# Optimization experiments

Hardware: AMD Instinct MI355X
Metric: run time of the kernel (lower is better)

## Reference

```python
import jax, jax.numpy as jnp
import numpy as np

B, LTMS, TTS, C_IN, F, H = 64, 16, 256, 128, 256, 256


def setup_inputs() -> dict:
    key = jax.random.key(0)
    ks = jax.random.split(key, 6)
    s = 0.05  # small init keeps relu-GRU numerically tame
    return {
        "x": jax.random.normal(ks[0], (B, LTMS * TTS, C_IN), dtype=jnp.float32),
        "conv_w": jax.random.normal(ks[1], (1, C_IN, F), dtype=jnp.float32) * s,
        "conv_b": jnp.zeros((F,), dtype=jnp.float32),
        "attn_w": jax.random.normal(ks[2], (TTS, TTS), dtype=jnp.float32) * s,
        "attn_b": jnp.zeros((TTS,), dtype=jnp.float32),
        "gru_w": jax.random.normal(ks[3], (F, 3 * H), dtype=jnp.float32) * s,
        "gru_u": jax.random.normal(ks[4], (H, 3 * H), dtype=jnp.float32) * s,
        "gru_b": jnp.zeros((2, 3 * H), dtype=jnp.float32),
    }


def _forward(x, conv_w, conv_b, attn_w, attn_b, gru_w, gru_u, gru_b):
    b = x.shape[0]
    # [B, LTMS*TTS, C] -> [B*LTMS, TTS, C]; segments are independent, so the
    # original per-segment Python loop vectorizes into the leading batch dim.
    xs = x.reshape(b * LTMS, TTS, C_IN)
    # Conv1D kernel_size=1 == pointwise GEMM, then ReLU (dropout=0 at inference)
    conv = jax.nn.relu(jnp.einsum('ntc,cf->ntf', xs, conv_w[0]) + conv_b)  # [N,T,F]
    # Attention: softmax(Dense) over time axis per filter, multiply back
    xt = conv.transpose(0, 2, 1)                                  # [N,F,T]
    probs = jax.nn.softmax(xt @ attn_w + attn_b, axis=-1)         # [N,F,T]
    x_att = conv * probs.transpose(0, 2, 1)                       # [N,T,F]
    # GRU (keras v2, reset_after=True), activation=relu, gate order z,r,h
    bi, br = gru_b[0], gru_b[1]
    gates_x = x_att @ gru_w + bi                                  # [N,T,3H]
    def step(h, gx):
        rec = h @ gru_u + br
        xz, xr, xh = jnp.split(gx, 3, axis=-1)
        rz, rr, rh = jnp.split(rec, 3, axis=-1)
        z = jax.nn.sigmoid(xz + rz)
        r = jax.nn.sigmoid(xr + rr)
        hh = jax.nn.relu(xh + r * rh)
        h_new = z * h + (1.0 - z) * hh
        return h_new, None
    h0 = jnp.zeros((b * LTMS, H), dtype=x.dtype)
    h_final, _ = jax.lax.scan(step, h0, gates_x.transpose(1, 0, 2))
    return h_final.reshape(b, LTMS, H)


def reference(x, conv_w, conv_b, attn_w, attn_b, gru_w, gru_u, gru_b):
    return _forward(x, conv_w, conv_b, attn_w, attn_b, gru_w, gru_u, gru_b)
```

## Files before the change

kernel.cpp:

```cpp
#include <hip/hip_runtime.h>
#include <stdint.h>

typedef unsigned short u16;
typedef __attribute__((ext_vector_type(8))) __bf16 bf16x8;
typedef __attribute__((ext_vector_type(8))) u16 u16x8;
typedef __attribute__((ext_vector_type(4))) float f32x4;

#define TTS 256
#define NSEG 1024
#define TC 32

__device__ __forceinline__ u16 f2bf(float f) {
  union { float f; uint32_t u; } v; v.f = f;
  uint32_t r = v.u + 0x7fffu + ((v.u >> 16) & 1u);
  return (u16)(r >> 16);
}
__device__ __forceinline__ float bf2f(u16 h) {
  union { uint32_t u; float f; } v; v.u = ((uint32_t)h) << 16;
  return v.f;
}
__device__ __forceinline__ float sigm(float x) {
  return __builtin_amdgcn_rcpf(1.0f + __expf(-x));
}
__device__ __forceinline__ void gl16(const void* g, void* l) {
  __builtin_amdgcn_global_load_lds(
      (const __attribute__((address_space(1))) unsigned int*)g,
      (__attribute__((address_space(3))) unsigned int*)l, 16, 0, 0);
}

__global__ void k_transp4(const float* __restrict__ cw, const float* __restrict__ aw,
                          const float* __restrict__ gw, const float* __restrict__ gu,
                          u16* __restrict__ cwT, u16* __restrict__ awT,
                          u16* __restrict__ gwT, u16* __restrict__ guT) {
  int b = blockIdx.x;
  const float* in; u16* out; int R, C, base;
  if (b < 128)       { in = cw; out = cwT; R = 128; C = 256; base = 0; }
  else if (b < 384)  { in = aw; out = awT; R = 256; C = 256; base = 128; }
  else if (b < 1152) { in = gw; out = gwT; R = 256; C = 768; base = 384; }
  else               { in = gu; out = guT; R = 256; C = 768; base = 1152; }
  int i = (b - base) * 256 + threadIdx.x;
  if (i < R * C) {
    int r = i / C, c = i % C;
    out[(size_t)c * R + r] = f2bf(in[i]);
  }
}

template <bool RELU, bool STORE_T, int AMODE>
__global__ __launch_bounds__(512, 2) void k_gemm(
    const void* __restrict__ Av, const u16* __restrict__ Bt,
    const float* __restrict__ bias, u16* __restrict__ out, int K, int Nld, int t0) {
  __shared__ __attribute__((aligned(16))) u16 ldsA[2][4096];
  __shared__ __attribute__((aligned(16))) u16 ldsB[2][8192];
  const int tid  = threadIdx.x;
  const int w    = tid >> 6;
  const int lane = tid & 63;
  const int quad = lane >> 4;
  const int l16  = lane & 15;
  const int m0 = blockIdx.x * 128;
  const int n0 = blockIdx.y * 256;
  const int wm = w >> 2, wn = w & 3;
  const int arow = tid & 127, ac = tid >> 7;
  const float* Af = (const float*)Av;
  const u16*   Ax = (const u16*)Av;

  f32x4 acc[4][4];
#pragma unroll
  for (int i = 0; i < 4; i++)
#pragma unroll
    for (int j = 0; j < 4; j++) acc[i][j] = f32x4{0.f, 0.f, 0.f, 0.f};

  float4 p0, p1;
  if (AMODE == 0) {
    const float* p = Af + (size_t)(m0 + arow) * K + ac * 8;
    p0 = *(const float4*)p;
    p1 = *(const float4*)(p + 4);
  } else {
    int r = m0 + arow, kk = ac * 8;
    gl16(Ax + (size_t)(r >> 5) * 65536 + (size_t)(kk >> 6) * 16384 +
             (t0 + (r & 31)) * 64 + (kk & 63),
         &ldsA[0][tid * 8]);
  }
#pragma unroll
  for (int i = 0; i < 2; i++) {
    int idx = i * 512 + tid, brow = idx & 255, bc = idx >> 8;
    gl16(Bt + (size_t)(n0 + brow) * K + bc * 8, &ldsB[0][idx * 8]);
  }
  if (AMODE == 0) {
    *(ushort4*)&ldsA[0][tid * 8]     = ushort4{f2bf(p0.x), f2bf(p0.y), f2bf(p0.z), f2bf(p0.w)};
    *(ushort4*)&ldsA[0][tid * 8 + 4] = ushort4{f2bf(p1.x), f2bf(p1.y), f2bf(p1.z), f2bf(p1.w)};
  }
  __syncthreads();

  int cur = 0;
  for (int k0 = 0; k0 < K; k0 += 32) {
    const int kn = k0 + 32;
    const bool more = kn < K;
    float4 q0, q1;
    if (more) {
      if (AMODE == 0) {
        const float* p = Af + (size_t)(m0 + arow) * K + kn + ac * 8;
        q0 = *(const float4*)p;
        q1 = *(const float4*)(p + 4);
      } else {
        int r = m0 + arow, kk = kn + ac * 8;
        gl16(Ax + (size_t)(r >> 5) * 65536 + (size_t)(kk >> 6) * 16384 +
                 (t0 + (r & 31)) * 64 + (kk & 63),
             &ldsA[cur ^ 1][tid * 8]);
      }
#pragma unroll
      for (int i = 0; i < 2; i++) {
        int idx = i * 512 + tid, brow = idx & 255, bc = idx >> 8;
        gl16(Bt + (size_t)(n0 + brow) * K + kn + bc * 8, &ldsB[cur ^ 1][idx * 8]);
      }
    }
    bf16x8 a[4], b[4];
#pragma unroll
    for (int i = 0; i < 4; i++)
      a[i] = *(const bf16x8*)&ldsA[cur][(quad * 128 + wm * 64 + i * 16 + l16) * 8];
#pragma unroll
    for (int j = 0; j < 4; j++)
      b[j] = *(const bf16x8*)&ldsB[cur][(quad * 256 + wn * 64 + j * 16 + l16) * 8];
#pragma unroll
    for (int i = 0; i < 4; i++)
#pragma unroll
      for (int j = 0; j < 4; j++)
        acc[i][j] = __builtin_amdgcn_mfma_f32_16x16x32_bf16(a[i], b[j], acc[i][j], 0, 0, 0);
    if (AMODE == 0 && more) {
      *(ushort4*)&ldsA[cur ^ 1][tid * 8]     = ushort4{f2bf(q0.x), f2bf(q0.y), f2bf(q0.z), f2bf(q0.w)};
      *(ushort4*)&ldsA[cur ^ 1][tid * 8 + 4] = ushort4{f2bf(q1.x), f2bf(q1.y), f2bf(q1.z), f2bf(q1.w)};
    }
    __syncthreads();
    cur ^= 1;
  }

#pragma unroll
  for (int j = 0; j < 4; j++) {
    int col = n0 + wn * 64 + j * 16 + l16;
    float bv = bias[col];
#pragma unroll
    for (int i = 0; i < 4; i++) {
      int row0 = m0 + wm * 64 + i * 16 + quad * 4;
      if (STORE_T) {
        int nseg = row0 >> 8, tt0 = row0 & 255;
        ushort4 o;
        float v0 = acc[i][j][0] + bv, v1 = acc[i][j][1] + bv;
        float v2 = acc[i][j][2] + bv, v3 = acc[i][j][3] + bv;
        if (RELU) {
          v0 = fmaxf(v0, 0.f); v1 = fmaxf(v1, 0.f);
          v2 = fmaxf(v2, 0.f); v3 = fmaxf(v3, 0.f);
        }
        o.x = f2bf(v0); o.y = f2bf(v1); o.z = f2bf(v2); o.w = f2bf(v3);
        *(ushort4*)&out[(size_t)nseg * 65536 + (size_t)(col >> 6) * 16384 +
                        (col & 63) * 256 + tt0] = o;
      } else {
#pragma unroll
        for (int r = 0; r < 4; r++) {
          float v = acc[i][j][r] + bv;
          if (RELU) v = fmaxf(v, 0.f);
          out[(size_t)(row0 + r) * Nld + col] = f2bf(v);
        }
      }
    }
  }
}

__global__ __launch_bounds__(256, 3) void k_attn(
    u16* xac,
    const u16* __restrict__ Wt,
    const float* __restrict__ attn_b) {
  __shared__ u16 ldsC[16384];
  __shared__ float redmax[4][64];
  __shared__ float redsum[4][64];
  __shared__ __attribute__((aligned(16))) u16 xbuf[4][16][76];
  const int tid  = threadIdx.x;
  const int w    = tid >> 6;
  const int lane = tid & 63;
  const int quad = lane >> 4;
  const int l16  = lane & 15;
  const int seg = blockIdx.x;
  const int c4  = blockIdx.y;
  u16* reg = xac + (size_t)seg * 65536 + (size_t)c4 * 16384;

  {
    const int f = tid & 63, g = tid >> 6;
#pragma unroll
    for (int u = 0; u < 8; u++) {
      int tch = g * 8 + u;
      *(bf16x8*)&ldsC[(tch * 64 + f) * 8] =
          *(const bf16x8*)(reg + (size_t)f * 256 + tch * 8);
    }
  }
  __syncthreads();

  f32x4 acc[4][4];
#pragma unroll
  for (int i = 0; i < 4; i++)
#pragma unroll
    for (int j = 0; j < 4; j++) acc[i][j] = f32x4{0.f, 0.f, 0.f, 0.f};

#pragma unroll
  for (int s = 0; s < 8; s++) {
    int k0 = s * 32;
    bf16x8 a[4], b[4];
#pragma unroll
    for (int i = 0; i < 4; i++)
      a[i] = *(const bf16x8*)(Wt + (size_t)(w * 64 + i * 16 + l16) * 256 + k0 + quad * 8);
#pragma unroll
    for (int j = 0; j < 4; j++)
      b[j] = *(const bf16x8*)&ldsC[((s * 4 + quad) * 64 + j * 16 + l16) * 8];
#pragma unroll
    for (int i = 0; i < 4; i++)
#pragma unroll
      for (int j = 0; j < 4; j++)
        acc[i][j] = __builtin_amdgcn_mfma_f32_16x16x32_bf16(a[i], b[j], acc[i][j], 0, 0, 0);
  }

#pragma unroll
  for (int i = 0; i < 4; i++)
#pragma unroll
    for (int r = 0; r < 4; r++) {
      float ab = attn_b[w * 64 + i * 16 + quad * 4 + r];
#pragma unroll
      for (int j = 0; j < 4; j++) acc[i][j][r] += ab;
    }

  float lmax[4];
#pragma unroll
  for (int j = 0; j < 4; j++) {
    float m = -1e30f;
#pragma unroll
    for (int i = 0; i < 4; i++)
#pragma unroll
      for (int r = 0; r < 4; r++) m = fmaxf(m, acc[i][j][r]);
    m = fmaxf(m, __shfl_xor(m, 16));
    m = fmaxf(m, __shfl_xor(m, 32));
    lmax[j] = m;
  }
  if (quad == 0) {
#pragma unroll
    for (int j = 0; j < 4; j++) redmax[w][j * 16 + l16] = lmax[j];
  }
  __syncthreads();
  float gmax[4];
#pragma unroll
  for (int j = 0; j < 4; j++) {
    int c = j * 16 + l16;
    gmax[j] = fmaxf(fmaxf(redmax[0][c], redmax[1][c]), fmaxf(redmax[2][c], redmax[3][c]));
  }
  float lsum[4];
#pragma unroll
  for (int j = 0; j < 4; j++) {
    float sacc = 0.f;
#pragma unroll
    for (int i = 0; i < 4; i++)
#pragma unroll
      for (int r = 0; r < 4; r++) {
        float e = __expf(acc[i][j][r] - gmax[j]);
        acc[i][j][r] = e;
        sacc += e;
      }
    sacc += __shfl_xor(sacc, 16);
    sacc += __shfl_xor(sacc, 32);
    lsum[j] = sacc;
  }
  if (quad == 0) {
#pragma unroll
    for (int j = 0; j < 4; j++) redsum[w][j * 16 + l16] = lsum[j];
  }
  __syncthreads();
  float rinv[4];
#pragma unroll
  for (int j = 0; j < 4; j++) {
    int c = j * 16 + l16;
    rinv[j] = 1.0f / (redsum[0][c] + redsum[1][c] + redsum[2][c] + redsum[3][c]);
  }

#pragma unroll
  for (int i = 0; i < 4; i++) {
#pragma unroll
    for (int r = 0; r < 4; r++) {
      int tp = w * 64 + i * 16 + quad * 4 + r;
#pragma unroll
      for (int j = 0; j < 4; j++) {
        int fl = j * 16 + l16;
        float cv = bf2f(ldsC[((tp >> 3) * 64 + fl) * 8 + (tp & 7)]);
        float xa = acc[i][j][r] * rinv[j] * cv;
        xbuf[w][quad * 4 + r][fl] = f2bf(xa);
      }
    }
    int rr = lane >> 2, oc = lane & 3;
    u16x8 v0 = *(const u16x8*)&xbuf[w][rr][oc * 16];
    u16x8 v1 = *(const u16x8*)&xbuf[w][rr][oc * 16 + 8];
    int tpb = w * 64 + i * 16 + rr;
    *(u16x8*)&reg[(size_t)tpb * 64 + oc * 16]     = v0;
    *(u16x8*)&reg[(size_t)tpb * 64 + oc * 16 + 8] = v1;
  }
}

__global__ __launch_bounds__(512) __attribute__((amdgpu_waves_per_eu(2, 2)))
void k_scan(
    const u16* __restrict__ gc,
    const u16* __restrict__ Ut,
    const float* __restrict__ br,
    float* __restrict__ hio,
    int init) {
  __shared__ __attribute__((aligned(16))) u16 hbT[2][4096];
  __shared__ __attribute__((aligned(16))) u16 ldsG[2][12288];
  const int tid  = threadIdx.x;
  const int w    = tid >> 6;
  const int lane = tid & 63;
  const int quad = lane >> 4;
  const int l16  = lane & 15;
  const int n0 = blockIdx.x * 16;
  const int cg[2] = {w, 8 + w};

  bf16x8 U[2][3][8];
#pragma unroll
  for (int grp = 0; grp < 2; grp++)
#pragma unroll
    for (int g = 0; g < 3; g++)
#pragma unroll
      for (int s = 0; s < 8; s++) {
        U[grp][g][s] = *(const bf16x8*)(Ut + (size_t)(g * 256 + cg[grp] * 16 + l16) * 256 + s * 32 + quad * 8);
        asm volatile("" : "+v"(U[grp][g][s]));
      }

  float brZ[2], brR[2], brH[2];
#pragma unroll
  for (int grp = 0; grp < 2; grp++) {
    int c = cg[grp] * 16 + l16;
    brZ[grp] = br[c]; brR[grp] = br[256 + c]; brH[grp] = br[512 + c];
  }

  int gbase[2], hwb[2];
#pragma unroll
  for (int grp = 0; grp < 2; grp++) {
    gbase[grp] = cg[grp] * 256 + quad * 16 + l16;
    int c = cg[grp] * 16 + l16;
    hwb[grp] = (c >> 5) * 512 + ((c >> 3) & 3) * 128 + (c & 7) + quad * 32;
  }
  const int ahb = quad * 128 + l16 * 8;

  float hreg[2][4];
#pragma unroll
  for (int grp = 0; grp < 2; grp++)
#pragma unroll
    for (int r = 0; r < 4; r++) {
      hreg[grp][r] = init ? 0.f
                          : hio[(size_t)(n0 + quad * 4 + r) * 256 + cg[grp] * 16 + l16];
      hbT[0][hwb[grp] + r * 8] = f2bf(hreg[grp][r]);
    }

  const u16* sp[3];
#pragma unroll
  for (int k = 0; k < 3; k++) {
    int id = tid + k * 512;
    int a = id & 1, q = (id >> 1) & 3, r = (id >> 3) & 3;
    int cgv = (id >> 5) & 15, g = id >> 9;
    sp[k] = gc + ((size_t)(n0 + q * 4 + r) * 32 + 0) * 768 + g * 256 + cgv * 16 + a * 8;
  }
#pragma unroll
  for (int k = 0; k < 3; k++) {
    gl16(sp[k], &ldsG[0][(tid + k * 512) * 8]);
    sp[k] += 768;
  }
  __syncthreads();

  for (int tt = 0; tt < TC; tt++) {
    if (tt + 1 < TC) {
#pragma unroll
      for (int k = 0; k < 3; k++) {
        gl16(sp[k], &ldsG[(tt + 1) & 1][(tid + k * 512) * 8]);
        sp[k] += 768;
      }
    }

    f32x4 acc[2][3];
#pragma unroll
    for (int grp = 0; grp < 2; grp++)
#pragma unroll
      for (int g = 0; g < 3; g++) acc[grp][g] = f32x4{0.f, 0.f, 0.f, 0.f};

    const u16* hR = hbT[tt & 1];
#pragma unroll
    for (int s = 0; s < 8; s++) {
      bf16x8 ah = *(const bf16x8*)&hR[ahb + s * 512];
#pragma unroll
      for (int grp = 0; grp < 2; grp++)
#pragma unroll
        for (int g = 0; g < 3; g++)
          acc[grp][g] = __builtin_amdgcn_mfma_f32_16x16x32_bf16(ah, U[grp][g][s], acc[grp][g], 0, 0, 0);
    }

    const u16* G = ldsG[tt & 1];
    u16* hW = hbT[(tt + 1) & 1];
#pragma unroll
    for (int grp = 0; grp < 2; grp++)
#pragma unroll
      for (int r = 0; r < 4; r++) {
        float gz = bf2f(G[gbase[grp] + 0 * 4096 + r * 64]);
        float gr = bf2f(G[gbase[grp] + 1 * 4096 + r * 64]);
        float gh = bf2f(G[gbase[grp] + 2 * 4096 + r * 64]);
        float z  = sigm(acc[grp][0][r] + gz + brZ[grp]);
        float rg = sigm(acc[grp][1][r] + gr + brR[grp]);
        float hh = fmaxf(gh + rg * (acc[grp][2][r] + brH[grp]), 0.f);
        float hn = z * hreg[grp][r] + (1.0f - z) * hh;
        hreg[grp][r] = hn;
        hW[hwb[grp] + r * 8] = f2bf(hn);
      }
    __syncthreads();
  }

#pragma unroll
  for (int grp = 0; grp < 2; grp++)
#pragma unroll
    for (int r = 0; r < 4; r++)
      hio[(size_t)(n0 + quad * 4 + r) * 256 + cg[grp] * 16 + l16] = hreg[grp][r];
}

extern "C" void kernel_launch(void* const* d_in, const int* in_sizes, int n_in,
                              void* d_out, int out_size, void* d_ws, size_t ws_size,
                              hipStream_t stream) {
  (void)in_sizes; (void)n_in; (void)out_size;
  const float* x      = (const float*)d_in[0];
  const float* conv_w = (const float*)d_in[1];
  const float* conv_b = (const float*)d_in[2];
  const float* attn_w = (const float*)d_in[3];
  const float* attn_b = (const float*)d_in[4];
  const float* gru_w  = (const float*)d_in[5];
  const float* gru_u  = (const float*)d_in[6];
  const float* gru_b  = (const float*)d_in[7];

  const size_t NEEDED = 185532416;
  if (ws_size < NEEDED) return;
  char* ws = (char*)d_ws;
  u16* xac     = (u16*)(ws);
  u16* gatesC  = (u16*)(ws + 134217728);
  u16* conv_wT = (u16*)(ws + 184549376);
  u16* attn_wT = (u16*)(ws + 184614912);
  u16* gru_wT  = (u16*)(ws + 184745984);
  u16* gru_uT  = (u16*)(ws + 185139200);

  hipLaunchKernelGGL(k_transp4, dim3(1920), dim3(256), 0, stream,
                     conv_w, attn_w, gru_w, gru_u, conv_wT, attn_wT, gru_wT, gru_uT);

  hipLaunchKernelGGL((k_gemm<true, true, 0>), dim3(2048, 1), dim3(512), 0, stream,
                     (const void*)x, conv_wT, conv_b, xac, 128, 0, 0);
  hipLaunchKernelGGL(k_attn, dim3(1024, 4), dim3(256), 0, stream,
                     xac, attn_wT, attn_b);
  for (int c = 0; c < 8; c++) {
    hipLaunchKernelGGL((k_gemm<false, false, 1>), dim3(256, 3), dim3(512), 0, stream,
                       (const void*)xac, gru_wT, gru_b, gatesC, 256, 768, c * TC);
    hipLaunchKernelGGL(k_scan, dim3(64), dim3(512), 0, stream,
                       gatesC, gru_uT, gru_b + 768, (float*)d_out, c == 0 ? 1 : 0);
  }
}
```

Baseline: 1.223 ms.

## Swizzle GEMM and attention LDS layouts and stage transposed epilogue stores through LDS

Changes the GEMM's LDS tile layout to row-major with an XOR swizzle, so global loads read contiguous k-chunks per row and fragment reads avoid bank conflicts. The transposed-store epilogue now goes through a per-wave LDS buffer, so each lane writes 16-byte vectors along time instead of scattered 8-byte pieces. The attention kernel loads its conv tile with direct global-to-LDS copies into an XOR-swizzled layout and reads fragments from that layout. This adds LDS usage and extra shuffling work in the epilogue.

```diff
diff --git a/kernel.cpp b/kernel.cpp
--- a/kernel.cpp
+++ b/kernel.cpp
@@ -51,6 +51,7 @@
     const float* __restrict__ bias, u16* __restrict__ out, int K, int Nld, int t0) {
   __shared__ __attribute__((aligned(16))) u16 ldsA[2][4096];
   __shared__ __attribute__((aligned(16))) u16 ldsB[2][8192];
+  __shared__ __attribute__((aligned(16))) u16 xw[STORE_T ? 8 * 16 * 70 : 16];
   const int tid  = threadIdx.x;
   const int w    = tid >> 6;
   const int lane = tid & 63;
@@ -59,7 +60,10 @@
   const int m0 = blockIdx.x * 128;
   const int n0 = blockIdx.y * 256;
   const int wm = w >> 2, wn = w & 3;
-  const int arow = tid & 127, ac = tid >> 7;
+  const int srow = tid >> 2;
+  const int scs  = (tid & 3) ^ (srow & 3);
+  const int aslot = (srow * 4 + scs) * 8;
+  const int xsw  = (quad ^ (l16 & 3)) * 8;
   const float* Af = (const float*)Av;
   const u16*   Ax = (const u16*)Av;
 
@@ -71,23 +75,24 @@
 
   float4 p0, p1;
   if (AMODE == 0) {
-    const float* p = Af + (size_t)(m0 + arow) * K + ac * 8;
+    const float* p = Af + (size_t)(m0 + srow) * K + (tid & 3) * 8;
     p0 = *(const float4*)p;
     p1 = *(const float4*)(p + 4);
   } else {
-    int r = m0 + arow, kk = ac * 8;
+    int r = m0 + srow, kk = scs * 8;
     gl16(Ax + (size_t)(r >> 5) * 65536 + (size_t)(kk >> 6) * 16384 +
              (t0 + (r & 31)) * 64 + (kk & 63),
          &ldsA[0][tid * 8]);
   }
 #pragma unroll
   for (int i = 0; i < 2; i++) {
-    int idx = i * 512 + tid, brow = idx & 255, bc = idx >> 8;
-    gl16(Bt + (size_t)(n0 + brow) * K + bc * 8, &ldsB[0][idx * 8]);
+    int idx = i * 512 + tid, brow = idx >> 2;
+    int bcs = (idx & 3) ^ (brow & 3);
+    gl16(Bt + (size_t)(n0 + brow) * K + bcs * 8, &ldsB[0][idx * 8]);
   }
   if (AMODE == 0) {
-    *(ushort4*)&ldsA[0][tid * 8]     = ushort4{f2bf(p0.x), f2bf(p0.y), f2bf(p0.z), f2bf(p0.w)};
-    *(ushort4*)&ldsA[0][tid * 8 + 4] = ushort4{f2bf(p1.x), f2bf(p1.y), f2bf(p1.z), f2bf(p1.w)};
+    *(ushort4*)&ldsA[0][aslot]     = ushort4{f2bf(p0.x), f2bf(p0.y), f2bf(p0.z), f2bf(p0.w)};
+    *(ushort4*)&ldsA[0][aslot + 4] = ushort4{f2bf(p1.x), f2bf(p1.y), f2bf(p1.z), f2bf(p1.w)};
   }
   __syncthreads();
 
@@ -98,61 +103,75 @@
     float4 q0, q1;
     if (more) {
       if (AMODE == 0) {
-        const float* p = Af + (size_t)(m0 + arow) * K + kn + ac * 8;
+        const float* p = Af + (size_t)(m0 + srow) * K + kn + (tid & 3) * 8;
         q0 = *(const float4*)p;
         q1 = *(const float4*)(p + 4);
       } else {
-        int r = m0 + arow, kk = kn + ac * 8;
+        int r = m0 + srow, kk = kn + scs * 8;
         gl16(Ax + (size_t)(r >> 5) * 65536 + (size_t)(kk >> 6) * 16384 +
                  (t0 + (r & 31)) * 64 + (kk & 63),
              &ldsA[cur ^ 1][tid * 8]);
       }
 #pragma unroll
       for (int i = 0; i < 2; i++) {
-        int idx = i * 512 + tid, brow = idx & 255, bc = idx >> 8;
-        gl16(Bt + (size_t)(n0 + brow) * K + kn + bc * 8, &ldsB[cur ^ 1][idx * 8]);
+        int idx = i * 512 + tid, brow = idx >> 2;
+        int bcs = (idx & 3) ^ (brow & 3);
+        gl16(Bt + (size_t)(n0 + brow) * K + kn + bcs * 8, &ldsB[cur ^ 1][idx * 8]);
       }
     }
     bf16x8 a[4], b[4];
 #pragma unroll
     for (int i = 0; i < 4; i++)
-      a[i] = *(const bf16x8*)&ldsA[cur][(quad * 128 + wm * 64 + i * 16 + l16) * 8];
+      a[i] = *(const bf16x8*)&ldsA[cur][(wm * 64 + i * 16 + l16) * 32 + xsw];
 #pragma unroll
     for (int j = 0; j < 4; j++)
-      b[j] = *(const bf16x8*)&ldsB[cur][(quad * 256 + wn * 64 + j * 16 + l16) * 8];
+      b[j] = *(const bf16x8*)&ldsB[cur][(wn * 64 + j * 16 + l16) * 32 + xsw];
 #pragma unroll
     for (int i = 0; i < 4; i++)
 #pragma unroll
       for (int j = 0; j < 4; j++)
         acc[i][j] = __builtin_amdgcn_mfma_f32_16x16x32_bf16(a[i], b[j], acc[i][j], 0, 0, 0);
     if (AMODE == 0 && more) {
-      *(ushort4*)&ldsA[cur ^ 1][tid * 8]     = ushort4{f2bf(q0.x), f2bf(q0.y), f2bf(q0.z), f2bf(q0.w)};
-      *(ushort4*)&ldsA[cur ^ 1][tid * 8 + 4] = ushort4{f2bf(q1.x), f2bf(q1.y), f2bf(q1.z), f2bf(q1.w)};
+      *(ushort4*)&ldsA[cur ^ 1][aslot]     = ushort4{f2bf(q0.x), f2bf(q0.y), f2bf(q0.z), f2bf(q0.w)};
+      *(ushort4*)&ldsA[cur ^ 1][aslot + 4] = ushort4{f2bf(q1.x), f2bf(q1.y), f2bf(q1.z), f2bf(q1.w)};
     }
     __syncthreads();
     cur ^= 1;
   }
 
-#pragma unroll
-  for (int j = 0; j < 4; j++) {
-    int col = n0 + wn * 64 + j * 16 + l16;
-    float bv = bias[col];
-#pragma unroll
-    for (int i = 0; i < 4; i++) {
-      int row0 = m0 + wm * 64 + i * 16 + quad * 4;
-      if (STORE_T) {
-        int nseg = row0 >> 8, tt0 = row0 & 255;
-        ushort4 o;
-        float v0 = acc[i][j][0] + bv, v1 = acc[i][j][1] + bv;
-        float v2 = acc[i][j][2] + bv, v3 = acc[i][j][3] + bv;
-        if (RELU) {
-          v0 = fmaxf(v0, 0.f); v1 = fmaxf(v1, 0.f);
-          v2 = fmaxf(v2, 0.f); v3 = fmaxf(v3, 0.f);
+  if (STORE_T) {
+    const int nseg = m0 >> 8;
+    const int ttw  = (m0 & 255) + wm * 64;
+    const int col16 = lane >> 2, part = lane & 3;
+    u16* xwp = &xw[w * 16 * 70];
+#pragma unroll
+    for (int j = 0; j < 4; j++) {
+      int col = n0 + wn * 64 + j * 16 + l16;
+      float bv = bias[col];
+#pragma unroll
+      for (int i = 0; i < 4; i++)
+#pragma unroll
+        for (int r = 0; r < 4; r++) {
+          float v = acc[i][j][r] + bv;
+          if (RELU) v = fmaxf(v, 0.f);
+          xwp[l16 * 70 + i * 16 + quad * 4 + r] = f2bf(v);
         }
-        o.x = f2bf(v0); o.y = f2bf(v1); o.z = f2bf(v2); o.w = f2bf(v3);
-        *(ushort4*)&out[(size_t)nseg * 65536 + (size_t)(col >> 6) * 16384 +
-                        (col & 63) * 256 + tt0] = o;
-      } else {
+      u16x8 v0 = *(const u16x8*)&xwp[col16 * 70 + part * 16];
+      u16x8 v1 = *(const u16x8*)&xwp[col16 * 70 + part * 16 + 8];
+      int colS = n0 + wn * 64 + j * 16 + col16;
+      size_t ob = (size_t)nseg * 65536 + (size_t)(colS >> 6) * 16384 +
+                  (size_t)(colS & 63) * 256 + ttw + part * 16;
+      *(u16x8*)&out[ob]     = v0;
+      *(u16x8*)&out[ob + 8] = v1;
+    }
+  } else {
+#pragma unroll
+    for (int j = 0; j < 4; j++) {
+      int col = n0 + wn * 64 + j * 16 + l16;
+      float bv = bias[col];
+#pragma unroll
+      for (int i = 0; i < 4; i++) {
+        int row0 = m0 + wm * 64 + i * 16 + quad * 4;
 #pragma unroll
         for (int r = 0; r < 4; r++) {
           float v = acc[i][j][r] + bv;
@@ -168,7 +187,7 @@
     u16* xac,
     const u16* __restrict__ Wt,
     const float* __restrict__ attn_b) {
-  __shared__ u16 ldsC[16384];
+  __shared__ __attribute__((aligned(16))) u16 ldsC[16384];
   __shared__ float redmax[4][64];
   __shared__ float redsum[4][64];
   __shared__ __attribute__((aligned(16))) u16 xbuf[4][16][76];
@@ -181,14 +200,11 @@
   const int c4  = blockIdx.y;
   u16* reg = xac + (size_t)seg * 65536 + (size_t)c4 * 16384;
 
-  {
-    const int f = tid & 63, g = tid >> 6;
-#pragma unroll
-    for (int u = 0; u < 8; u++) {
-      int tch = g * 8 + u;
-      *(bf16x8*)&ldsC[(tch * 64 + f) * 8] =
-          *(const bf16x8*)(reg + (size_t)f * 256 + tch * 8);
-    }
+#pragma unroll
+  for (int u = 0; u < 8; u++) {
+    int id = u * 256 + tid;
+    int f = id >> 5;
+    gl16(reg + ((id * 8) ^ ((f & 7) << 3)), &ldsC[id * 8]);
   }
   __syncthreads();
 
@@ -206,8 +222,10 @@
     for (int i = 0; i < 4; i++)
       a[i] = *(const bf16x8*)(Wt + (size_t)(w * 64 + i * 16 + l16) * 256 + k0 + quad * 8);
 #pragma unroll
-    for (int j = 0; j < 4; j++)
-      b[j] = *(const bf16x8*)&ldsC[((s * 4 + quad) * 64 + j * 16 + l16) * 8];
+    for (int j = 0; j < 4; j++) {
+      int fl = j * 16 + l16;
+      b[j] = *(const bf16x8*)&ldsC[(fl * 256 + s * 32 + quad * 8) ^ ((fl & 7) << 3)];
+    }
 #pragma unroll
     for (int i = 0; i < 4; i++)
 #pragma unroll
@@ -283,7 +301,7 @@
 #pragma unroll
       for (int j = 0; j < 4; j++) {
         int fl = j * 16 + l16;
-        float cv = bf2f(ldsC[((tp >> 3) * 64 + fl) * 8 + (tp & 7)]);
+        float cv = bf2f(ldsC[(fl * 256 + tp) ^ ((fl & 7) << 3)]);
         float xa = acc[i][j][r] * rinv[j] * cv;
         xbuf[w][quad * 4 + r][fl] = f2bf(xa);
       }
```

Measured after the change: 1.122 ms. 8.3% less time.
